# Performance work log

Measured on AMD Instinct MI355X. Metric: run time of the kernel, lower is better.

The kernel has to match this reference:

```python
import jax, jax.numpy as jnp
import numpy as np

N = 4096   # num_agents
F = 512    # feat_dim
P = 512    # phi_dim
A = 512    # aggr_dim
S = 6      # state_dim
H = 20     # MLP hidden width (hidden_layers=(20,20))


def _lstm(X, wih, whh, b):
    # torch.nn.LSTM single layer on an unbatched sequence X: [T, in] -> [T, hidden]
    pre = X @ wih + b  # [T, 4*hidden]
    Fh = whh.shape[0]
    def step(carry, p):
        h, c = carry
        g = p + h @ whh
        i, f, gg, o = jnp.split(g, 4, axis=-1)  # torch gate order: i, f, g, o
        c = jax.nn.sigmoid(f) * c + jax.nn.sigmoid(i) * jnp.tanh(gg)
        h = jax.nn.sigmoid(o) * jnp.tanh(c)
        return (h, c), h
    init = (jnp.zeros((Fh,), X.dtype), jnp.zeros((Fh,), X.dtype))
    _, hs = jax.lax.scan(step, init, pre)
    return hs


def setup_inputs():
    key = jax.random.key(0)
    ks = jax.random.split(key, 30)
    def rn(k, shape, s=0.05):
        return (jax.random.normal(k, shape) * s).astype(jnp.float32)
    x = jax.random.normal(ks[0], (N, F), dtype=jnp.float32)
    states = jax.random.normal(ks[1], (N, S), dtype=jnp.float32)
    # one comm link per agent (E == N, required by update()'s concat with x)
    src = jax.random.randint(ks[2], (N,), 0, N)
    dst = jnp.arange(N)
    inp = dict(x=x, states=states, src=src, dst=dst)
    inp["phi_w0"] = rn(ks[3], (4, F + S, H)); inp["phi_b0"] = rn(ks[4], (4, H))
    inp["phi_w1"] = rn(ks[5], (4, H, H));     inp["phi_b1"] = rn(ks[6], (4, H))
    inp["phi_w2"] = rn(ks[7], (4, H, P));     inp["phi_b2"] = rn(ks[8], (4, P))
    inp["tq_w"] = rn(ks[9], (4, P, A));  inp["tq_b"] = rn(ks[10], (4, A))
    inp["tk_w"] = rn(ks[11], (4, P, A)); inp["tk_b"] = rn(ks[12], (4, A))
    inp["tv_w"] = rn(ks[13], (4, P, A)); inp["tv_b"] = rn(ks[14], (4, A))
    inp["ts_w"] = rn(ks[15], (4, P, A)); inp["ts_b"] = rn(ks[16], (4, A))
    inp["wih0"] = rn(ks[17], (4, A + F, 4 * F)); inp["whh0"] = rn(ks[18], (4, F, 4 * F))
    inp["b0"] = rn(ks[19], (4, 4 * F))
    inp["wih1"] = rn(ks[20], (4, F, 4 * F)); inp["whh1"] = rn(ks[21], (4, F, 4 * F))
    inp["b1"] = rn(ks[22], (4, 4 * F))
    inp["cbf_w"] = rn(ks[23], (F, 1)); inp["cbf_b"] = rn(ks[24], (1,))
    return inp


def reference(x, states, src, dst, phi_w0, phi_b0, phi_w1, phi_b1, phi_w2, phi_b2,
              tq_w, tq_b, tk_w, tk_b, tv_w, tv_b, ts_w, ts_b,
              wih0, whh0, b0, wih1, whh1, b1, cbf_w, cbf_b):
    inv_sqrt_a = 1.0 / jnp.sqrt(jnp.float32(A))

    def gnn_layer(l, xin):
        # message: phi(concat(x_j, states_j - states_i))  (j = src, i = dst)
        msg = jnp.concatenate([xin[src], states[src] - states[dst]], axis=1)  # [E, F+S]
        h = jax.nn.relu(msg @ phi_w0[l] + phi_b0[l])
        h = jax.nn.relu(h @ phi_w1[l] + phi_b1[l])
        phi = h @ phi_w2[l] + phi_b2[l]  # [E, P]
        # aggregate: TransformerConv over message rows (E == N), heads=1
        q = phi @ tq_w[l] + tq_b[l]
        k = phi @ tk_w[l] + tk_b[l]
        v = phi @ tv_w[l] + tv_b[l]
        logits = jnp.sum(q[dst] * k[src], axis=-1) * inv_sqrt_a  # [E]
        m = jax.ops.segment_max(logits, dst, num_segments=N)
        e = jnp.exp(logits - m[dst])
        ssum = jax.ops.segment_sum(e, dst, num_segments=N)
        alpha = e / ssum[dst]
        aggr = jax.ops.segment_sum(alpha[:, None] * v[src], dst, num_segments=N)
        aggr = aggr + phi @ ts_w[l] + ts_b[l]  # root/skip connection
        # update: 2-layer LSTM over agents as an unbatched sequence
        gi = jnp.concatenate([aggr, xin], axis=1)  # [N, A+F]
        h0 = _lstm(gi, wih0[l], whh0[l], b0[l])
        h1 = _lstm(h0, wih1[l], whh1[l], b1[l])
        return h1

    xcur = gnn_layer(0, x)
    xcur = jax.nn.relu(xcur)
    xcur = gnn_layer(1, xcur)
    xcur = gnn_layer(2, xcur)      # feat_transformer layer 1
    xcur = jax.nn.relu(xcur)
    xcur = gnn_layer(3, xcur)      # feat_transformer layer 2
    hcbf = jax.nn.relu(xcur) @ cbf_w + cbf_b  # feat_2_CBF
    return xcur, hcbf
```

## Files before the change

### kernel.cpp

```cpp
#include <hip/hip_runtime.h>
#include <hip/hip_bf16.h>
#include <math.h>

#define NA   4096
#define FDIM 512
#define SDIM 6
#define HID  20
#define GDIM 2048
#define LWG  32

__device__ __forceinline__ float sigf(float x) { return 1.0f / (1.0f + __expf(-x)); }
__device__ __forceinline__ float tanh_fast(float x) {
    float e = __expf(2.0f * x);
    return 1.0f - 2.0f / (e + 1.0f);
}

__device__ __forceinline__ void atomicMaxF(float* addr, float v) {
    if (v >= 0.0f) atomicMax((int*)addr, __float_as_int(v));
    else           atomicMin((unsigned int*)addr, __float_as_uint(v));
}

__global__ void phi_fused(const float* __restrict__ xin, const float* __restrict__ states,
                          const int* __restrict__ src, const int* __restrict__ dst,
                          const float* __restrict__ w0, const float* __restrict__ b0,
                          const float* __restrict__ w1, const float* __restrict__ b1,
                          const float* __restrict__ w2, const float* __restrict__ b2,
                          float* __restrict__ phi)
{
    int e = blockIdx.x, tid = threadIdx.x;
    __shared__ float msgv[FDIM + SDIM];
    __shared__ float hb1[HID];
    __shared__ float hb2[HID];
    int s = src[e], d = dst[e];
    for (int i = tid; i < FDIM; i += 64) msgv[i] = xin[(size_t)s * FDIM + i];
    if (tid < SDIM) msgv[FDIM + tid] = states[s * SDIM + tid] - states[d * SDIM + tid];
    __syncthreads();
    if (tid < HID) {
        float acc = b0[tid];
        for (int k = 0; k < FDIM + SDIM; k++) acc += msgv[k] * w0[k * HID + tid];
        hb1[tid] = fmaxf(acc, 0.0f);
    }
    __syncthreads();
    if (tid < HID) {
        float acc = b1[tid];
        for (int k = 0; k < HID; k++) acc += hb1[k] * w1[k * HID + tid];
        hb2[tid] = fmaxf(acc, 0.0f);
    }
    __syncthreads();
    for (int c = tid; c < FDIM; c += 64) {
        float acc = b2[c];
        for (int k = 0; k < HID; k++) acc += hb2[k] * w2[k * FDIM + c];
        phi[(size_t)e * FDIM + c] = acc;
    }
}

__global__ void __launch_bounds__(256)
gemm64(const float* __restrict__ A1, int lda1,
       const float* __restrict__ A2, int lda2, int splitA,
       const float* __restrict__ B, const float* __restrict__ bias,
       float* __restrict__ C, int M, int N, int K)
{
    __shared__ float a_lds[16][64];
    __shared__ float b_lds[16][64];
    int tid = threadIdx.x;
    int m0 = blockIdx.y * 64, n0 = blockIdx.x * 64;
    int tr = tid >> 2, tc4 = (tid & 3) * 4;
    int bry = tid >> 4, bc4 = (tid & 15) * 4;
    int ty = tid >> 4, tx = tid & 15;
    float acc[4][4] = {};

    for (int kt = 0; kt < K; kt += 16) {
        int ak = kt + tc4;
        const float* arow;
        int acol;
        if (ak < splitA) { arow = A1 + (size_t)(m0 + tr) * lda1; acol = ak; }
        else             { arow = A2 + (size_t)(m0 + tr) * lda2; acol = ak - splitA; }
        float4 av = *(const float4*)(arow + acol);
        a_lds[tc4 + 0][tr] = av.x;
        a_lds[tc4 + 1][tr] = av.y;
        a_lds[tc4 + 2][tr] = av.z;
        a_lds[tc4 + 3][tr] = av.w;
        float4 bv = *(const float4*)(B + (size_t)(kt + bry) * N + n0 + bc4);
        *(float4*)&b_lds[bry][bc4] = bv;
        __syncthreads();
#pragma unroll
        for (int kk = 0; kk < 16; kk++) {
            float4 a = *(const float4*)&a_lds[kk][ty * 4];
            float4 b = *(const float4*)&b_lds[kk][tx * 4];
            acc[0][0] += a.x * b.x; acc[0][1] += a.x * b.y; acc[0][2] += a.x * b.z; acc[0][3] += a.x * b.w;
            acc[1][0] += a.y * b.x; acc[1][1] += a.y * b.y; acc[1][2] += a.y * b.z; acc[1][3] += a.y * b.w;
            acc[2][0] += a.z * b.x; acc[2][1] += a.z * b.y; acc[2][2] += a.z * b.z; acc[2][3] += a.z * b.w;
            acc[3][0] += a.w * b.x; acc[3][1] += a.w * b.y; acc[3][2] += a.w * b.z; acc[3][3] += a.w * b.w;
        }
        __syncthreads();
    }
    float4 bb = *(const float4*)(bias + n0 + tx * 4);
#pragma unroll
    for (int i = 0; i < 4; i++) {
        int row = m0 + ty * 4 + i;
        float4 o;
        o.x = acc[i][0] + bb.x; o.y = acc[i][1] + bb.y; o.z = acc[i][2] + bb.z; o.w = acc[i][3] + bb.w;
        *(float4*)&C[(size_t)row * N + n0 + tx * 4] = o;
    }
}

__global__ void att_init(float* __restrict__ m, float* __restrict__ ssum)
{
    int i = blockIdx.x * blockDim.x + threadIdx.x;
    if (i < NA) { m[i] = -INFINITY; ssum[i] = 0.0f; }
}

__global__ void att_logits(const float* __restrict__ q, const float* __restrict__ k,
                           const int* __restrict__ src, const int* __restrict__ dst,
                           float* __restrict__ logits, float* __restrict__ m)
{
    int e = blockIdx.x, tid = threadIdx.x;
    int s = src[e], d = dst[e];
    const float4* qr = (const float4*)(q + (size_t)d * FDIM);
    const float4* kr = (const float4*)(k + (size_t)s * FDIM);
    float acc = 0.0f;
    for (int i = tid; i < FDIM / 4; i += 64) {
        float4 a = qr[i], b = kr[i];
        acc += a.x * b.x + a.y * b.y + a.z * b.z + a.w * b.w;
    }
    for (int off = 32; off; off >>= 1) acc += __shfl_down(acc, off);
    if (tid == 0) {
        float v = acc * 0.04419417382415922f;
        logits[e] = v;
        atomicMaxF(&m[d], v);
    }
}

__global__ void att_expsum(const float* __restrict__ logits, const float* __restrict__ m,
                           const int* __restrict__ dst,
                           float* __restrict__ ebuf, float* __restrict__ ssum)
{
    int e = blockIdx.x * blockDim.x + threadIdx.x;
    if (e < NA) {
        float v = __expf(logits[e] - m[dst[e]]);
        ebuf[e] = v;
        atomicAdd(&ssum[dst[e]], v);
    }
}

__global__ void att_scatter(const float* __restrict__ v, const int* __restrict__ src,
                            const int* __restrict__ dst, const float* __restrict__ ebuf,
                            const float* __restrict__ ssum, float* __restrict__ aggr)
{
    int e = blockIdx.x, tid = threadIdx.x;
    int s = src[e], d = dst[e];
    float alpha = ebuf[e] / ssum[d];
    const float* vr = v + (size_t)s * FDIM;
    float* ar = aggr + (size_t)d * FDIM;
    for (int c = tid; c < FDIM; c += 256) atomicAdd(&ar[c], alpha * vr[c]);
}

__global__ void __launch_bounds__(512, 2)
lstm_pair(const float* __restrict__ pre0, const float* __restrict__ whh0,
          const float* __restrict__ wih1, const float* __restrict__ whh1,
          const float* __restrict__ b1,
          float* __restrict__ xout,
          unsigned long long* __restrict__ hfull,
          unsigned long long* __restrict__ hbuf1,
          unsigned int tag0, unsigned int tag1, int T)
{
    const int wg = blockIdx.x;
    const bool roleB = wg >= LWG;
    const int w = wg & (LWG - 1);
    const int tid = threadIdx.x;
    const int dl = tid & 15;
    const int gate = (tid >> 4) & 3;
    const int seg = tid >> 6;
    const int j = gate * 512 + w * 16 + dl;

    float wreg[128];
    if (!roleB) {
        const float* wc = whh0 + (size_t)(seg * 64) * GDIM + j;
#pragma unroll
        for (int kk = 0; kk < 64; kk++) wreg[kk] = wc[(size_t)kk * GDIM];
    } else {
        const float* wc = (seg < 4)
            ? (wih1 + (size_t)(seg * 128) * GDIM + j)
            : (whh1 + (size_t)((seg - 4) * 128) * GDIM + j);
#pragma unroll
        for (int kk = 0; kk < 128; kk++) wreg[kk] = wc[(size_t)kk * GDIM];
    }

    __shared__ float h_lds[1024];
    __shared__ float red[512];
    __shared__ float gbuf[64];
    float c = 0.0f;
    float extra = 0.0f;
    if (tid < 64) extra = roleB ? b1[j] : pre0[j];
    if (!roleB) h_lds[tid] = 0.0f;
    else        h_lds[512 + tid] = 0.0f;
    __syncthreads();

    if (!roleB) {
        for (int t = 0; t < T; t++) {
            const float* hseg = h_lds + seg * 64;
            float a0 = 0, a1 = 0, a2 = 0, a3 = 0;
#pragma unroll
            for (int kk = 0; kk < 64; kk += 4) {
                float4 hv = *(const float4*)(hseg + kk);
                a0 += wreg[kk + 0] * hv.x;
                a1 += wreg[kk + 1] * hv.y;
                a2 += wreg[kk + 2] * hv.z;
                a3 += wreg[kk + 3] * hv.w;
            }
            red[tid] = (a0 + a1) + (a2 + a3);
            __syncthreads();
            if (tid < 64) {
                float tot = extra;
#pragma unroll
                for (int s = 0; s < 8; s++) tot += red[tid + 64 * s];
                gbuf[tid] = tot;
                if (t + 1 < T) extra = pre0[(size_t)(t + 1) * GDIM + j];
            }
            __syncthreads();
            if (tid < 16) {
                float ii = gbuf[tid], ff = gbuf[16 + tid], gg = gbuf[32 + tid], oo = gbuf[48 + tid];
                c = sigf(ff) * c + sigf(ii) * tanh_fast(gg);
                float h = sigf(oo) * tanh_fast(c);
                unsigned long long word =
                    ((unsigned long long)(tag0 + (unsigned)t + 1u) << 32) |
                    (unsigned long long)__float_as_uint(h);
                __hip_atomic_store(&hfull[(size_t)t * 512 + w * 16 + tid], word,
                                   __ATOMIC_RELAXED, __HIP_MEMORY_SCOPE_AGENT);
            }
            if (t + 1 < T) {
                unsigned long long want = tag0 + (unsigned)t + 1u;
                const unsigned long long* p = &hfull[(size_t)t * 512 + tid];
                unsigned long long v = __hip_atomic_load(p, __ATOMIC_RELAXED, __HIP_MEMORY_SCOPE_AGENT);
                while ((v >> 32) != want)
                    v = __hip_atomic_load(p, __ATOMIC_RELAXED, __HIP_MEMORY_SCOPE_AGENT);
                h_lds[tid] = __uint_as_float((unsigned)v);
                __syncthreads();
            }
        }
    } else {
        for (int t = 0; t < T; t++) {
            {
                unsigned long long want = tag0 + (unsigned)t + 1u;
                const unsigned long long* p = &hfull[(size_t)t * 512 + tid];
                unsigned long long v = __hip_atomic_load(p, __ATOMIC_RELAXED, __HIP_MEMORY_SCOPE_AGENT);
                while ((v >> 32) != want)
                    v = __hip_atomic_load(p, __ATOMIC_RELAXED, __HIP_MEMORY_SCOPE_AGENT);
                h_lds[tid] = __uint_as_float((unsigned)v);
            }
            __syncthreads();
            const float* hseg = h_lds + seg * 128;
            float a0 = 0, a1 = 0, a2 = 0, a3 = 0;
#pragma unroll
            for (int kk = 0; kk < 128; kk += 4) {
                float4 hv = *(const float4*)(hseg + kk);
                a0 += wreg[kk + 0] * hv.x;
                a1 += wreg[kk + 1] * hv.y;
                a2 += wreg[kk + 2] * hv.z;
                a3 += wreg[kk + 3] * hv.w;
            }
            red[tid] = (a0 + a1) + (a2 + a3);
            __syncthreads();
            if (tid < 64) {
                float tot = extra;
#pragma unroll
                for (int s = 0; s < 8; s++) tot += red[tid + 64 * s];
                gbuf[tid] = tot;
            }
            __syncthreads();
            if (tid < 16) {
                float ii = gbuf[tid], ff = gbuf[16 + tid], gg = gbuf[32 + tid], oo = gbuf[48 + tid];
                c = sigf(ff) * c + sigf(ii) * tanh_fast(gg);
                float h = sigf(oo) * tanh_fast(c);
                xout[(size_t)t * 512 + w * 16 + tid] = h;
                unsigned long long word =
                    ((unsigned long long)(tag1 + (unsigned)t + 1u) << 32) |
                    (unsigned long long)__float_as_uint(h);
                __hip_atomic_store(&hbuf1[(t & 1) * 512 + w * 16 + tid], word,
                                   __ATOMIC_RELAXED, __HIP_MEMORY_SCOPE_AGENT);
            }
            if (t + 1 < T) {
                unsigned long long want = tag1 + (unsigned)t + 1u;
                const unsigned long long* p = &hbuf1[(t & 1) * 512 + tid];
                unsigned long long v = __hip_atomic_load(p, __ATOMIC_RELAXED, __HIP_MEMORY_SCOPE_AGENT);
                while ((v >> 32) != want)
                    v = __hip_atomic_load(p, __ATOMIC_RELAXED, __HIP_MEMORY_SCOPE_AGENT);
                h_lds[512 + tid] = __uint_as_float((unsigned)v);
                __syncthreads();
            }
        }
    }
}

__global__ void relu_ip(float* __restrict__ x, int n)
{
    int i = blockIdx.x * blockDim.x + threadIdx.x;
    if (i < n) x[i] = fmaxf(x[i], 0.0f);
}

__global__ void cbf_head(const float* __restrict__ xc, const float* __restrict__ w,
                         const float* __restrict__ b, float* __restrict__ out)
{
    int i = blockIdx.x, tid = threadIdx.x;
    const float* xr = xc + (size_t)i * FDIM;
    float acc = 0.0f;
    for (int d = tid; d < FDIM; d += 64) acc += fmaxf(xr[d], 0.0f) * w[d];
    for (int off = 32; off; off >>= 1) acc += __shfl_down(acc, off);
    if (tid == 0) out[i] = acc + b[0];
}

__global__ void zero_u64(unsigned long long* __restrict__ p, int n)
{
    int i = blockIdx.x * blockDim.x + threadIdx.x;
    int stride = gridDim.x * blockDim.x;
    for (; i < n; i += stride) p[i] = 0ull;
}

extern "C" void kernel_launch(void* const* d_in, const int* in_sizes, int n_in,
                              void* d_out, int out_size, void* d_ws, size_t ws_size,
                              hipStream_t stream)
{
    const float* x      = (const float*)d_in[0];
    const float* states = (const float*)d_in[1];
    const int*   src    = (const int*)d_in[2];
    const int*   dst    = (const int*)d_in[3];
    const float* phi_w0 = (const float*)d_in[4];
    const float* phi_b0 = (const float*)d_in[5];
    const float* phi_w1 = (const float*)d_in[6];
    const float* phi_b1 = (const float*)d_in[7];
    const float* phi_w2 = (const float*)d_in[8];
    const float* phi_b2 = (const float*)d_in[9];
    const float* tq_w = (const float*)d_in[10]; const float* tq_b = (const float*)d_in[11];
    const float* tk_w = (const float*)d_in[12]; const float* tk_b = (const float*)d_in[13];
    const float* tv_w = (const float*)d_in[14]; const float* tv_b = (const float*)d_in[15];
    const float* ts_w = (const float*)d_in[16]; const float* ts_b = (const float*)d_in[17];
    const float* wih0 = (const float*)d_in[18]; const float* whh0 = (const float*)d_in[19];
    const float* b0   = (const float*)d_in[20];
    const float* wih1 = (const float*)d_in[21]; const float* whh1 = (const float*)d_in[22];
    const float* b1   = (const float*)d_in[23];
    const float* cbf_w = (const float*)d_in[24]; const float* cbf_b = (const float*)d_in[25];

    float* ws = (float*)d_ws;
    size_t off = 0;
    auto alloc = [&](size_t n) { float* p = ws + off; off += n; return p; };
    float* xA     = alloc((size_t)NA * FDIM);
    float* xB     = alloc((size_t)NA * FDIM);
    float* phi    = alloc((size_t)NA * FDIM);
    float* qb     = alloc((size_t)NA * FDIM);
    float* kb     = alloc((size_t)NA * FDIM);
    float* vb     = alloc((size_t)NA * FDIM);
    float* aggr   = alloc((size_t)NA * FDIM);
    float* pre    = alloc((size_t)NA * GDIM);
    float* logits = alloc(NA);
    float* mb     = alloc(NA);
    float* ssum   = alloc(NA);
    float* ebuf   = alloc(NA);
    const int HFULL_WORDS = NA * 512;
    unsigned long long* hfull = (unsigned long long*)alloc((size_t)2 * (HFULL_WORDS + 1024));
    unsigned long long* hbuf1 = hfull + HFULL_WORDS;

    float* out_x   = (float*)d_out;
    float* out_cbf = out_x + (size_t)NA * FDIM;

    zero_u64<<<2048, 256, 0, stream>>>(hfull, HFULL_WORDS + 1024);

    dim3 g512(FDIM / 64, NA / 64);
    dim3 g2048(GDIM / 64, NA / 64);

    const float* xin = x;
    for (int l = 0; l < 4; l++) {
        float* xout = (l == 3) ? out_x : ((l & 1) ? xB : xA);

        phi_fused<<<NA, 64, 0, stream>>>(xin, states, src, dst,
            phi_w0 + (size_t)l * 518 * HID, phi_b0 + l * HID,
            phi_w1 + (size_t)l * HID * HID, phi_b1 + l * HID,
            phi_w2 + (size_t)l * HID * FDIM, phi_b2 + l * FDIM, phi);

        gemm64<<<g512, 256, 0, stream>>>(phi, FDIM, phi, FDIM, FDIM,
            tq_w + (size_t)l * FDIM * FDIM, tq_b + l * FDIM, qb, NA, FDIM, FDIM);
        gemm64<<<g512, 256, 0, stream>>>(phi, FDIM, phi, FDIM, FDIM,
            tk_w + (size_t)l * FDIM * FDIM, tk_b + l * FDIM, kb, NA, FDIM, FDIM);
        gemm64<<<g512, 256, 0, stream>>>(phi, FDIM, phi, FDIM, FDIM,
            tv_w + (size_t)l * FDIM * FDIM, tv_b + l * FDIM, vb, NA, FDIM, FDIM);
        gemm64<<<g512, 256, 0, stream>>>(phi, FDIM, phi, FDIM, FDIM,
            ts_w + (size_t)l * FDIM * FDIM, ts_b + l * FDIM, aggr, NA, FDIM, FDIM);

        att_init<<<NA / 256, 256, 0, stream>>>(mb, ssum);
        att_logits<<<NA, 64, 0, stream>>>(qb, kb, src, dst, logits, mb);
        att_expsum<<<NA / 256, 256, 0, stream>>>(logits, mb, dst, ebuf, ssum);
        att_scatter<<<NA, 256, 0, stream>>>(vb, src, dst, ebuf, ssum, aggr);

        gemm64<<<g2048, 256, 0, stream>>>(aggr, FDIM, xin, FDIM, FDIM,
            wih0 + (size_t)l * 1024 * GDIM, b0 + (size_t)l * GDIM, pre, NA, GDIM, 1024);

        lstm_pair<<<2 * LWG, 512, 0, stream>>>(pre,
            whh0 + (size_t)l * FDIM * GDIM,
            wih1 + (size_t)l * FDIM * GDIM,
            whh1 + (size_t)l * FDIM * GDIM,
            b1 + (size_t)l * GDIM,
            xout, hfull, hbuf1,
            (unsigned)(2 * l) * NA, (unsigned)(2 * l + 1) * NA, NA);

        if (l == 0 || l == 2)
            relu_ip<<<(NA * FDIM + 255) / 256, 256, 0, stream>>>(xout, NA * FDIM);
        xin = xout;
    }

    cbf_head<<<NA, 64, 0, stream>>>(out_x, cbf_w, cbf_b, out_cbf);
}
```

Measured before the change: 38.76 ms.

## Use 128x128 GEMM tiles, batch QKVS projections, widen phi MLP parallelism

Replaces the 64x64 fp32 GEMM with a 128x128 tile version that computes 8x8 outputs per thread, and batches the four q/k/v/skip projections into one launch using blockIdx.z to select the weight pointers. The phi MLP kernel now runs 256 threads per edge and splits the first-layer reduction into 12 partial sums per hidden unit. The aim is more arithmetic per LDS load, fewer launches, and less serial work in the phi layer. In exchange the kernel uses more registers, which can lower occupancy, and the 4096x2048 GEMM now launches fewer blocks.

```diff
diff --git a/kernel.cpp b/kernel.cpp
--- a/kernel.cpp
+++ b/kernel.cpp
@@ -20,87 +20,137 @@
     else           atomicMin((unsigned int*)addr, __float_as_uint(v));
 }
 
-__global__ void phi_fused(const float* __restrict__ xin, const float* __restrict__ states,
-                          const int* __restrict__ src, const int* __restrict__ dst,
-                          const float* __restrict__ w0, const float* __restrict__ b0,
-                          const float* __restrict__ w1, const float* __restrict__ b1,
-                          const float* __restrict__ w2, const float* __restrict__ b2,
-                          float* __restrict__ phi)
+__global__ void __launch_bounds__(256)
+phi_fused(const float* __restrict__ xin, const float* __restrict__ states,
+          const int* __restrict__ src, const int* __restrict__ dst,
+          const float* __restrict__ w0, const float* __restrict__ b0,
+          const float* __restrict__ w1, const float* __restrict__ b1,
+          const float* __restrict__ w2, const float* __restrict__ b2,
+          float* __restrict__ phi)
 {
     int e = blockIdx.x, tid = threadIdx.x;
     __shared__ float msgv[FDIM + SDIM];
+    __shared__ float red[240];
     __shared__ float hb1[HID];
     __shared__ float hb2[HID];
     int s = src[e], d = dst[e];
-    for (int i = tid; i < FDIM; i += 64) msgv[i] = xin[(size_t)s * FDIM + i];
+    for (int i = tid; i < FDIM; i += 256) msgv[i] = xin[(size_t)s * FDIM + i];
     if (tid < SDIM) msgv[FDIM + tid] = states[s * SDIM + tid] - states[d * SDIM + tid];
     __syncthreads();
-    if (tid < HID) {
-        float acc = b0[tid];
-        for (int k = 0; k < FDIM + SDIM; k++) acc += msgv[k] * w0[k * HID + tid];
-        hb1[tid] = fmaxf(acc, 0.0f);
+    if (tid < 240) {
+        int col = tid / 12, sg = tid % 12;
+        int k0 = sg * 44, k1 = min(FDIM + SDIM, k0 + 44);
+        float acc = 0.0f;
+        for (int k = k0; k < k1; k++) acc += msgv[k] * w0[k * HID + col];
+        red[tid] = acc;
     }
     __syncthreads();
     if (tid < HID) {
-        float acc = b1[tid];
-        for (int k = 0; k < HID; k++) acc += hb1[k] * w1[k * HID + tid];
-        hb2[tid] = fmaxf(acc, 0.0f);
+        float a = b0[tid];
+#pragma unroll
+        for (int q = 0; q < 12; q++) a += red[tid * 12 + q];
+        hb1[tid] = fmaxf(a, 0.0f);
     }
     __syncthreads();
-    for (int c = tid; c < FDIM; c += 64) {
-        float acc = b2[c];
-        for (int k = 0; k < HID; k++) acc += hb2[k] * w2[k * FDIM + c];
-        phi[(size_t)e * FDIM + c] = acc;
-    }
-}
+    if (tid < HID) {
+        float a = b1[tid];
+#pragma unroll
+        for (int k = 0; k < HID; k++) a += hb1[k] * w1[k * HID + tid];
+        hb2[tid] = fmaxf(a, 0.0f);
+    }
+    __syncthreads();
+    for (int c = tid; c < FDIM; c += 256) {
+        float a = b2[c];
+#pragma unroll
+        for (int k = 0; k < HID; k++) a += hb2[k] * w2[k * FDIM + c];
+        phi[(size_t)e * FDIM + c] = a;
+    }
+}
+
+struct Ptrs4 {
+    const float* B[4];
+    const float* bias[4];
+    float* C[4];
+};
 
 __global__ void __launch_bounds__(256)
-gemm64(const float* __restrict__ A1, int lda1,
-       const float* __restrict__ A2, int lda2, int splitA,
-       const float* __restrict__ B, const float* __restrict__ bias,
-       float* __restrict__ C, int M, int N, int K)
-{
-    __shared__ float a_lds[16][64];
-    __shared__ float b_lds[16][64];
-    int tid = threadIdx.x;
-    int m0 = blockIdx.y * 64, n0 = blockIdx.x * 64;
-    int tr = tid >> 2, tc4 = (tid & 3) * 4;
-    int bry = tid >> 4, bc4 = (tid & 15) * 4;
-    int ty = tid >> 4, tx = tid & 15;
-    float acc[4][4] = {};
+gemm128(const float* __restrict__ A1, int lda1,
+        const float* __restrict__ A2, int lda2, int splitA,
+        Ptrs4 p, int M, int N, int K)
+{
+    __shared__ float a_lds[16][132];
+    __shared__ float b_lds[16][132];
+    const float* __restrict__ B    = p.B[blockIdx.z];
+    const float* __restrict__ bias = p.bias[blockIdx.z];
+    float* __restrict__ C          = p.C[blockIdx.z];
+    const int tid = threadIdx.x;
+    const int m0 = blockIdx.y * 128, n0 = blockIdx.x * 128;
+    const int ar = tid >> 2, ak4 = (tid & 3) * 4;
+    const int br = tid >> 5, bc4 = (tid & 31) * 4;
+    const int ty = tid >> 4, tx = tid & 15;
+    float acc[8][8] = {};
 
     for (int kt = 0; kt < K; kt += 16) {
-        int ak = kt + tc4;
-        const float* arow;
+        int ak = kt + ak4;
+        const float* abase;
         int acol;
-        if (ak < splitA) { arow = A1 + (size_t)(m0 + tr) * lda1; acol = ak; }
-        else             { arow = A2 + (size_t)(m0 + tr) * lda2; acol = ak - splitA; }
-        float4 av = *(const float4*)(arow + acol);
-        a_lds[tc4 + 0][tr] = av.x;
-        a_lds[tc4 + 1][tr] = av.y;
-        a_lds[tc4 + 2][tr] = av.z;
-        a_lds[tc4 + 3][tr] = av.w;
-        float4 bv = *(const float4*)(B + (size_t)(kt + bry) * N + n0 + bc4);
-        *(float4*)&b_lds[bry][bc4] = bv;
+        if (ak < splitA) { abase = A1; acol = ak;
+            const float* r0 = abase + (size_t)(m0 + ar) * lda1 + acol;
+            const float* r1 = abase + (size_t)(m0 + ar + 64) * lda1 + acol;
+            float4 a0 = *(const float4*)r0;
+            float4 a1 = *(const float4*)r1;
+            a_lds[ak4 + 0][ar] = a0.x; a_lds[ak4 + 1][ar] = a0.y;
+            a_lds[ak4 + 2][ar] = a0.z; a_lds[ak4 + 3][ar] = a0.w;
+            a_lds[ak4 + 0][ar + 64] = a1.x; a_lds[ak4 + 1][ar + 64] = a1.y;
+            a_lds[ak4 + 2][ar + 64] = a1.z; a_lds[ak4 + 3][ar + 64] = a1.w;
+        } else {
+            acol = ak - splitA;
+            const float* r0 = A2 + (size_t)(m0 + ar) * lda2 + acol;
+            const float* r1 = A2 + (size_t)(m0 + ar + 64) * lda2 + acol;
+            float4 a0 = *(const float4*)r0;
+            float4 a1 = *(const float4*)r1;
+            a_lds[ak4 + 0][ar] = a0.x; a_lds[ak4 + 1][ar] = a0.y;
+            a_lds[ak4 + 2][ar] = a0.z; a_lds[ak4 + 3][ar] = a0.w;
+            a_lds[ak4 + 0][ar + 64] = a1.x; a_lds[ak4 + 1][ar + 64] = a1.y;
+            a_lds[ak4 + 2][ar + 64] = a1.z; a_lds[ak4 + 3][ar + 64] = a1.w;
+        }
+        {
+            float4 b0v = *(const float4*)(B + (size_t)(kt + br) * N + n0 + bc4);
+            float4 b1v = *(const float4*)(B + (size_t)(kt + br + 8) * N + n0 + bc4);
+            *(float4*)&b_lds[br][bc4] = b0v;
+            *(float4*)&b_lds[br + 8][bc4] = b1v;
+        }
         __syncthreads();
 #pragma unroll
         for (int kk = 0; kk < 16; kk++) {
-            float4 a = *(const float4*)&a_lds[kk][ty * 4];
-            float4 b = *(const float4*)&b_lds[kk][tx * 4];
-            acc[0][0] += a.x * b.x; acc[0][1] += a.x * b.y; acc[0][2] += a.x * b.z; acc[0][3] += a.x * b.w;
-            acc[1][0] += a.y * b.x; acc[1][1] += a.y * b.y; acc[1][2] += a.y * b.z; acc[1][3] += a.y * b.w;
-            acc[2][0] += a.z * b.x; acc[2][1] += a.z * b.y; acc[2][2] += a.z * b.z; acc[2][3] += a.z * b.w;
-            acc[3][0] += a.w * b.x; acc[3][1] += a.w * b.y; acc[3][2] += a.w * b.z; acc[3][3] += a.w * b.w;
+            float av[8], bv[8];
+            *(float4*)&av[0] = *(const float4*)&a_lds[kk][ty * 4];
+            *(float4*)&av[4] = *(const float4*)&a_lds[kk][64 + ty * 4];
+            *(float4*)&bv[0] = *(const float4*)&b_lds[kk][tx * 4];
+            *(float4*)&bv[4] = *(const float4*)&b_lds[kk][64 + tx * 4];
+#pragma unroll
+            for (int i = 0; i < 8; i++)
+#pragma unroll
+                for (int j = 0; j < 8; j++)
+                    acc[i][j] += av[i] * bv[j];
         }
         __syncthreads();
     }
-    float4 bb = *(const float4*)(bias + n0 + tx * 4);
-#pragma unroll
-    for (int i = 0; i < 4; i++) {
-        int row = m0 + ty * 4 + i;
-        float4 o;
-        o.x = acc[i][0] + bb.x; o.y = acc[i][1] + bb.y; o.z = acc[i][2] + bb.z; o.w = acc[i][3] + bb.w;
-        *(float4*)&C[(size_t)row * N + n0 + tx * 4] = o;
+
+    float4 bb0 = *(const float4*)(bias + n0 + tx * 4);
+    float4 bb1 = *(const float4*)(bias + n0 + 64 + tx * 4);
+    const float bbs0[4] = { bb0.x, bb0.y, bb0.z, bb0.w };
+    const float bbs1[4] = { bb1.x, bb1.y, bb1.z, bb1.w };
+#pragma unroll
+    for (int i = 0; i < 8; i++) {
+        int row = m0 + ((i < 4) ? (ty * 4 + i) : (64 + ty * 4 + i - 4));
+        float4 o0, o1;
+        o0.x = acc[i][0] + bbs0[0]; o0.y = acc[i][1] + bbs0[1];
+        o0.z = acc[i][2] + bbs0[2]; o0.w = acc[i][3] + bbs0[3];
+        o1.x = acc[i][4] + bbs1[0]; o1.y = acc[i][5] + bbs1[1];
+        o1.z = acc[i][6] + bbs1[2]; o1.w = acc[i][7] + bbs1[3];
+        *(float4*)&C[(size_t)row * N + n0 + tx * 4] = o0;
+        *(float4*)&C[(size_t)row * N + n0 + 64 + tx * 4] = o1;
     }
 }
 
@@ -364,34 +414,39 @@
 
     zero_u64<<<2048, 256, 0, stream>>>(hfull, HFULL_WORDS + 1024);
 
-    dim3 g512(FDIM / 64, NA / 64);
-    dim3 g2048(GDIM / 64, NA / 64);
-
     const float* xin = x;
     for (int l = 0; l < 4; l++) {
         float* xout = (l == 3) ? out_x : ((l & 1) ? xB : xA);
 
-        phi_fused<<<NA, 64, 0, stream>>>(xin, states, src, dst,
+        phi_fused<<<NA, 256, 0, stream>>>(xin, states, src, dst,
             phi_w0 + (size_t)l * 518 * HID, phi_b0 + l * HID,
             phi_w1 + (size_t)l * HID * HID, phi_b1 + l * HID,
             phi_w2 + (size_t)l * HID * FDIM, phi_b2 + l * FDIM, phi);
 
-        gemm64<<<g512, 256, 0, stream>>>(phi, FDIM, phi, FDIM, FDIM,
-            tq_w + (size_t)l * FDIM * FDIM, tq_b + l * FDIM, qb, NA, FDIM, FDIM);
-        gemm64<<<g512, 256, 0, stream>>>(phi, FDIM, phi, FDIM, FDIM,
-            tk_w + (size_t)l * FDIM * FDIM, tk_b + l * FDIM, kb, NA, FDIM, FDIM);
-        gemm64<<<g512, 256, 0, stream>>>(phi, FDIM, phi, FDIM, FDIM,
-            tv_w + (size_t)l * FDIM * FDIM, tv_b + l * FDIM, vb, NA, FDIM, FDIM);
-        gemm64<<<g512, 256, 0, stream>>>(phi, FDIM, phi, FDIM, FDIM,
-            ts_w + (size_t)l * FDIM * FDIM, ts_b + l * FDIM, aggr, NA, FDIM, FDIM);
+        {
+            Ptrs4 p;
+            p.B[0] = tq_w + (size_t)l * FDIM * FDIM; p.bias[0] = tq_b + l * FDIM; p.C[0] = qb;
+            p.B[1] = tk_w + (size_t)l * FDIM * FDIM; p.bias[1] = tk_b + l * FDIM; p.C[1] = kb;
+            p.B[2] = tv_w + (size_t)l * FDIM * FDIM; p.bias[2] = tv_b + l * FDIM; p.C[2] = vb;
+            p.B[3] = ts_w + (size_t)l * FDIM * FDIM; p.bias[3] = ts_b + l * FDIM; p.C[3] = aggr;
+            gemm128<<<dim3(FDIM / 128, NA / 128, 4), 256, 0, stream>>>(
+                phi, FDIM, phi, FDIM, FDIM, p, NA, FDIM, FDIM);
+        }
 
         att_init<<<NA / 256, 256, 0, stream>>>(mb, ssum);
         att_logits<<<NA, 64, 0, stream>>>(qb, kb, src, dst, logits, mb);
         att_expsum<<<NA / 256, 256, 0, stream>>>(logits, mb, dst, ebuf, ssum);
         att_scatter<<<NA, 256, 0, stream>>>(vb, src, dst, ebuf, ssum, aggr);
 
-        gemm64<<<g2048, 256, 0, stream>>>(aggr, FDIM, xin, FDIM, FDIM,
-            wih0 + (size_t)l * 1024 * GDIM, b0 + (size_t)l * GDIM, pre, NA, GDIM, 1024);
+        {
+            Ptrs4 p;
+            p.B[0] = wih0 + (size_t)l * 1024 * GDIM; p.bias[0] = b0 + (size_t)l * GDIM; p.C[0] = pre;
+            p.B[1] = p.B[0]; p.bias[1] = p.bias[0]; p.C[1] = pre;
+            p.B[2] = p.B[0]; p.bias[2] = p.bias[0]; p.C[2] = pre;
+            p.B[3] = p.B[0]; p.bias[3] = p.bias[0]; p.C[3] = pre;
+            gemm128<<<dim3(GDIM / 128, NA / 128, 1), 256, 0, stream>>>(
+                aggr, FDIM, xin, FDIM, FDIM, p, NA, GDIM, 1024);
+        }
 
         lstm_pair<<<2 * LWG, 512, 0, stream>>>(pre,
             whh0 + (size_t)l * FDIM * GDIM,
```

Result: no change. 38.41 ms (-0.9%).
